# Performance work log

Hardware: AMD Instinct MI355X
Metric: run time of the kernel (lower is better)

Reference implementation:

```python
import jax, jax.numpy as jnp
import numpy as np

N = 50000     # nodes
E = 800000    # edges (avg degree 16)
IN = 128
HID = 128
OUT = 128


def _init_lin(key, n_out, n_in, bias=True):
    k1, k2 = jax.random.split(key)
    bound = 1.0 / np.sqrt(n_in)
    W = jax.random.uniform(k1, (n_out, n_in), minval=-bound, maxval=bound, dtype=jnp.float32)
    if bias:
        b = jax.random.uniform(k2, (n_out,), minval=-bound, maxval=bound, dtype=jnp.float32)
        return W, b
    return W


def setup_inputs() -> dict:
    key = jax.random.key(0)
    ks = jax.random.split(key, 20)
    inp = {
        "s": jax.random.normal(ks[0], (N, IN), dtype=jnp.float32),
        "t": jax.random.normal(ks[1], (N, IN), dtype=jnp.float32),
        "edge_index": jax.random.randint(ks[2], (2, E), 0, N, dtype=jnp.int64),
        "edge_weight": jax.random.normal(ks[3], (E,), dtype=jnp.float32),
    }
    dims = [(HID, IN), (OUT, HID)]
    i = 4
    for layer in range(2):
        n_out, n_in = dims[layer]
        for pre in ("s", "t"):
            Wl, bl = _init_lin(ks[i], n_out, n_in, bias=True); i += 1
            Wr = _init_lin(ks[i], n_out, n_in, bias=False); i += 1
            inp[f"{pre}{layer}_Wl"] = Wl
            inp[f"{pre}{layer}_bl"] = bl
            inp[f"{pre}{layer}_Wr"] = Wr
    return inp


def _sage(x, src, dst, w, Wl, bl, Wr):
    """SAGEConv (mean aggr, weighted messages): lin_l(mean_j w_ij x_j) + lin_r(x_i)."""
    n = x.shape[0]
    msg = x[src] * w[:, None]                                   # [E, d] gather
    agg = jax.ops.segment_sum(msg, dst, num_segments=n)         # [N, d] scatter-add
    cnt = jax.ops.segment_sum(jnp.ones_like(w), dst, num_segments=n)
    mean = agg / jnp.maximum(cnt, 1.0)[:, None]
    return mean @ Wl.T + bl + x @ Wr.T


def reference(s, t, edge_index, edge_weight,
              s0_Wl, s0_bl, s0_Wr, t0_Wl, t0_bl, t0_Wr,
              s1_Wl, s1_bl, s1_Wr, t1_Wl, t1_bl, t1_Wr):
    w = jax.nn.sigmoid(edge_weight)
    src, dst = edge_index[0], edge_index[1]
    # layer 0 (relu; dropout is identity in eval mode)
    s1 = jax.nn.relu(_sage(t, src, dst, w, s0_Wl, s0_bl, s0_Wr))
    t1 = jax.nn.relu(_sage(s, dst, src, w, t0_Wl, t0_bl, t0_Wr))  # flipped edges
    # layer 1 (no activation)
    s2 = _sage(t1, src, dst, w, s1_Wl, s1_bl, s1_Wr)
    t2 = _sage(s1, dst, src, w, t1_Wl, t1_bl, t1_Wr)
    return (s2, t2)
```

## Files before the change

### kernel.cpp

```cpp
#include <hip/hip_runtime.h>
#include <hip/hip_bf16.h>

#define DIM 128
#define BINSHIFT 8
#define BINSZ 256
#define MAXBINS2 400
#define EPB 2048

typedef __attribute__((ext_vector_type(4))) float f32x4;
typedef __attribute__((ext_vector_type(8))) short bf16x8;
typedef __attribute__((ext_vector_type(8))) unsigned short u16x8;

static __device__ __forceinline__ float b2f(unsigned short u) {
    return __uint_as_float(((unsigned int)u) << 16);
}
static __device__ __forceinline__ unsigned short f2b(float f) {
    unsigned int x = __float_as_uint(f);
    unsigned int r = (x + 0x7fffu + ((x >> 16) & 1u)) >> 16;
    return (unsigned short)r;
}

static __device__ __forceinline__ void fma8(float* acc, float w, uint4 v) {
    const unsigned int* u = &v.x;
#pragma unroll
    for (int k = 0; k < 4; k++) {
        acc[2 * k]     += w * __uint_as_float(u[k] << 16);
        acc[2 * k + 1] += w * __uint_as_float(u[k] & 0xffff0000u);
    }
}

__global__ __launch_bounds__(256) void dgnn_bincount(const int* __restrict__ srcI,
        const int* __restrict__ dstI, int* __restrict__ binCnt, int E, int NBINS) {
    __shared__ int hist[MAXBINS2];
    const int nb2 = 2 * NBINS;
    for (int i = threadIdx.x; i < nb2; i += 256) hist[i] = 0;
    __syncthreads();
    int base = blockIdx.x * EPB;
    int end = min(base + EPB, E);
    for (int e = base + threadIdx.x; e < end; e += 256) {
        atomicAdd(&hist[dstI[e] >> BINSHIFT], 1);
        atomicAdd(&hist[NBINS + (srcI[e] >> BINSHIFT)], 1);
    }
    __syncthreads();
    for (int i = threadIdx.x; i < nb2; i += 256) {
        int c = hist[i];
        if (c) atomicAdd(&binCnt[i], c);
    }
}

__global__ __launch_bounds__(1024) void dgnn_binscan(const int* __restrict__ binCnt,
        int* __restrict__ binOffs, int* __restrict__ binCur, int M) {
    __shared__ int sm[1024];
    int tid = threadIdx.x;
    int chunk = (M + 1023) / 1024;
    int b = tid * chunk, e = min(b + chunk, M);
    int s = 0;
    for (int i = b; i < e; i++) s += binCnt[i];
    sm[tid] = s;
    __syncthreads();
    for (int o = 1; o < 1024; o <<= 1) {
        int v = (tid >= o) ? sm[tid - o] : 0;
        __syncthreads();
        sm[tid] += v;
        __syncthreads();
    }
    int run = sm[tid] - s;
    for (int i = b; i < e; i++) {
        int c = binCnt[i];
        binOffs[i] = run; binCur[i] = run;
        run += c;
    }
    if (tid == 1023) binOffs[M] = run;
}

__global__ __launch_bounds__(256) void dgnn_binscatter(const float* __restrict__ ew,
        const int* __restrict__ srcI, const int* __restrict__ dstI,
        int* __restrict__ binCur, int2* __restrict__ binned, int E, int NBINS) {
    __shared__ int hist[MAXBINS2];
    const int nb2 = 2 * NBINS;
    for (int i = threadIdx.x; i < nb2; i += 256) hist[i] = 0;
    __syncthreads();
    int base = blockIdx.x * EPB;
    int end = min(base + EPB, E);
    for (int e = base + threadIdx.x; e < end; e += 256) {
        atomicAdd(&hist[dstI[e] >> BINSHIFT], 1);
        atomicAdd(&hist[NBINS + (srcI[e] >> BINSHIFT)], 1);
    }
    __syncthreads();
    for (int i = threadIdx.x; i < nb2; i += 256) {
        int c = hist[i];
        hist[i] = c ? atomicAdd(&binCur[i], c) : 0;
    }
    __syncthreads();
    for (int e = base + threadIdx.x; e < end; e += 256) {
        int d = dstI[e], s = srcI[e];
        float x = ew[e];
        float w = 1.0f / (1.0f + expf(-x));
        int wb = __float_as_int(w);
        int packed = d | (s << 16);
        int pd = atomicAdd(&hist[d >> BINSHIFT], 1);
        binned[pd] = make_int2(packed, wb);
        int ps = atomicAdd(&hist[NBINS + (s >> BINSHIFT)], 1);
        binned[ps] = make_int2(packed, wb);
    }
}

__global__ __launch_bounds__(256) void dgnn_csrfinal(const int2* __restrict__ binned,
        const int* __restrict__ binOffs, int* __restrict__ offsD, int* __restrict__ offsS,
        int2* __restrict__ nbr2D, int2* __restrict__ nbr2S, int E, int N, int NBINS) {
    int b = blockIdx.x;
    bool isD = b < NBINS;
    int nodeBase = (isD ? b : b - NBINS) << BINSHIFT;
    int beg = binOffs[b], end = binOffs[b + 1];
    int K = end - beg;
    int csrBase = isD ? beg : beg - E;
    int* offs = isD ? offsD : offsS;
    int2* out = isD ? nbr2D : nbr2S;

    __shared__ int cnt[BINSZ], cur[BINSZ], scanb[BINSZ];
    cnt[threadIdx.x] = 0;
    __syncthreads();
    for (int i = threadIdx.x; i < K; i += 256) {
        int pk = binned[beg + i].x;
        int node = isD ? (pk & 0xffff) : ((pk >> 16) & 0xffff);
        atomicAdd(&cnt[node - nodeBase], 1);
    }
    __syncthreads();
    int v = cnt[threadIdx.x];
    scanb[threadIdx.x] = v;
    __syncthreads();
#pragma unroll
    for (int o = 1; o < 256; o <<= 1) {
        int u = (threadIdx.x >= o) ? scanb[threadIdx.x - o] : 0;
        __syncthreads();
        scanb[threadIdx.x] += u;
        __syncthreads();
    }
    int pos = csrBase + scanb[threadIdx.x] - v;
    cur[threadIdx.x] = pos;
    int n = nodeBase + threadIdx.x;
    if (n < N) offs[n] = pos;
    __syncthreads();
    for (int i = threadIdx.x; i < K; i += 256) {
        int2 en = binned[beg + i];
        int node, nbr;
        if (isD) { node = en.x & 0xffff; nbr = (en.x >> 16) & 0xffff; }
        else     { node = (en.x >> 16) & 0xffff; nbr = en.x & 0xffff; }
        int p = atomicAdd(&cur[node - nodeBase], 1);
        out[p] = make_int2(nbr, en.y);
    }
    if (threadIdx.x == 0) {
        if (b == NBINS - 1) offsD[N] = E;
        if (b == 2 * NBINS - 1) offsS[N] = E;
    }
}

__global__ __launch_bounds__(256) void dgnn_cvt2(const float* __restrict__ s,
        const float* __restrict__ t, unsigned short* __restrict__ sb,
        unsigned short* __restrict__ tb, int n4, int halfb) {
    int which = (blockIdx.x >= halfb) ? 1 : 0;
    int i = (blockIdx.x - which * halfb) * 256 + threadIdx.x;
    if (i >= n4) return;
    const float* src = which ? t : s;
    unsigned short* dst = which ? tb : sb;
    float4 v = ((const float4*)src)[i];
    ushort4 o;
    o.x = f2b(v.x); o.y = f2b(v.y); o.z = f2b(v.z); o.w = f2b(v.w);
    ((ushort4*)dst)[i] = o;
}

struct WPtrs { const float* Wl[4]; const float* Wr[4]; };

__global__ __launch_bounds__(256) void dgnn_cvtw(WPtrs wp, unsigned short* __restrict__ Wc) {
    int tid = blockIdx.x * 256 + threadIdx.x;
    int i4 = tid << 2;
    int conv = i4 >> 15;
    int rem = i4 & 32767;
    int ch = rem >> 8;
    int k = rem & 255;
    const float* src = (k < 128) ? wp.Wl[conv] : wp.Wr[conv];
    float4 v = *(const float4*)(src + ch * DIM + (k & 127));
    ushort4 o;
    o.x = f2b(v.x); o.y = f2b(v.y); o.z = f2b(v.z); o.w = f2b(v.w);
    *(ushort4*)(Wc + i4) = o;
}

__global__ __launch_bounds__(256) void dgnn_gather2(
        const unsigned short* __restrict__ xbD, const int* __restrict__ offsD,
        const int2* __restrict__ nbrD, unsigned short* __restrict__ meanD,
        const unsigned short* __restrict__ xbS, const int* __restrict__ offsS,
        const int2* __restrict__ nbrS, unsigned short* __restrict__ meanS,
        int N, int halfb) {
    int which = (blockIdx.x >= halfb) ? 1 : 0;
    const unsigned short* xb = which ? xbS : xbD;
    const int* offs          = which ? offsS : offsD;
    const int2* nbr2         = which ? nbrS : nbrD;
    unsigned short* meanb    = which ? meanS : meanD;

    long long gid = (long long)(blockIdx.x - which * halfb) * 256 + threadIdx.x;
    int n = (int)(gid >> 5);
    if (n >= N) return;
    const int l32 = (int)gid & 31;
    const int q2  = l32 >> 4;
    const int m   = l32 & 15;

    int beg = offs[n], end = offs[n + 1];
    float acc[8];
#pragma unroll
    for (int k = 0; k < 8; k++) acc[k] = 0.f;

    for (int base = beg; base < end; base += 32) {
        int cnt = end - base; if (cnt > 32) cnt = 32;
        bool inb = (base + l32) < end;
        int2 gw = inb ? nbr2[base + l32] : make_int2(0, 0);
        int   g_l = gw.x;
        float w_l = __int_as_float(gw.y);

        int it = 0;
        for (; it + 8 <= cnt; it += 8) {
            int e0 = it + q2, e1 = it + 2 + q2, e2 = it + 4 + q2, e3 = it + 6 + q2;
            int g0 = __shfl(g_l, e0, 32), g1 = __shfl(g_l, e1, 32);
            int g2 = __shfl(g_l, e2, 32), g3 = __shfl(g_l, e3, 32);
            float w0 = __shfl(w_l, e0, 32), w1 = __shfl(w_l, e1, 32);
            float w2 = __shfl(w_l, e2, 32), w3 = __shfl(w_l, e3, 32);
            uint4 v0 = *(const uint4*)(xb + ((size_t)g0 << 7) + (m << 3));
            uint4 v1 = *(const uint4*)(xb + ((size_t)g1 << 7) + (m << 3));
            uint4 v2 = *(const uint4*)(xb + ((size_t)g2 << 7) + (m << 3));
            uint4 v3 = *(const uint4*)(xb + ((size_t)g3 << 7) + (m << 3));
            fma8(acc, w0, v0); fma8(acc, w1, v1);
            fma8(acc, w2, v2); fma8(acc, w3, v3);
        }
        for (; it < cnt; it += 2) {
            int e0 = it + q2;
            int g0 = __shfl(g_l, e0, 32);
            float w0 = __shfl(w_l, e0, 32);
            uint4 v0 = *(const uint4*)(xb + ((size_t)g0 << 7) + (m << 3));
            fma8(acc, w0, v0);
        }
    }

#pragma unroll
    for (int k = 0; k < 8; k++)
        acc[k] += __shfl_xor(acc[k], 16);

    if (q2 == 0) {
        float inv = 1.0f / fmaxf((float)(end - beg), 1.0f);
        u16x8 o;
#pragma unroll
        for (int k = 0; k < 8; k++) o[k] = f2b(acc[k] * inv);
        *(u16x8*)(meanb + ((size_t)n << 7) + (m << 3)) = o;
    }
}

__global__ __launch_bounds__(256) void dgnn_node2(
        const unsigned short* __restrict__ meanA, const unsigned short* __restrict__ xbA,
        const unsigned short* __restrict__ WcA, const float* __restrict__ biasA,
        float* __restrict__ outfA, unsigned short* __restrict__ outbA,
        const unsigned short* __restrict__ meanB, const unsigned short* __restrict__ xbB,
        const unsigned short* __restrict__ WcB, const float* __restrict__ biasB,
        float* __restrict__ outfB, unsigned short* __restrict__ outbB,
        int N, int mode, int halfb) {
    __shared__ __align__(16) unsigned short sW[128 * 256];

    int which = (blockIdx.x >= halfb) ? 1 : 0;
    const unsigned short* meanb = which ? meanB : meanA;
    const unsigned short* xb    = which ? xbB : xbA;
    const unsigned short* Wc    = which ? WcB : WcA;
    const float* bias           = which ? biasB : biasA;
    float* outf                 = which ? outfB : outfA;
    unsigned short* outb        = which ? outbB : outbA;
    int lb = blockIdx.x - which * halfb;

    for (int i = threadIdx.x; i < 4096; i += 256) {
        int ch = i >> 5;
        int off = (i & 31) << 4;
        float4 v = *(const float4*)((const char*)Wc + ((size_t)i << 4));
        int soff = off ^ ((ch & 7) << 4);
        *(float4*)((char*)sW + ch * 512 + soff) = v;
    }
    __syncthreads();

    const int wid = threadIdx.x >> 6;
    const int lane = threadIdx.x & 63;
    const int r = lane & 15;
    const int q = lane >> 4;
    const int ntiles = (N + 15) >> 4;

    for (int tile = lb * 4 + wid; tile < ntiles; tile += halfb * 4) {
        const int n0 = tile << 4;
        const unsigned short* A0 = meanb + (size_t)(n0 + r) * DIM + q * 8;
        const unsigned short* A1 = xb    + (size_t)(n0 + r) * DIM + q * 8;

        f32x4 acc[8];
#pragma unroll
        for (int ct = 0; ct < 8; ct++) acc[ct] = (f32x4){0.f, 0.f, 0.f, 0.f};

#pragma unroll
        for (int ks = 0; ks < 8; ks++) {
            bf16x8 a = (ks < 4) ? *(const bf16x8*)(A0 + ks * 32)
                                : *(const bf16x8*)(A1 + (ks - 4) * 32);
#pragma unroll
            for (int ct = 0; ct < 8; ct++) {
                int ch = ct * 16 + r;
                int soff = (ks * 64 + q * 16) ^ ((ch & 7) << 4);
                bf16x8 b = *(const bf16x8*)((const char*)sW + ch * 512 + soff);
                acc[ct] = __builtin_amdgcn_mfma_f32_16x16x32_bf16(a, b, acc[ct], 0, 0, 0);
            }
        }

#pragma unroll
        for (int ct = 0; ct < 8; ct++) {
            int ch = ct * 16 + r;
            float bv = bias[ch];
#pragma unroll
            for (int rr = 0; rr < 4; rr++) {
                int n = n0 + q * 4 + rr;
                if (n >= N) break;
                float v = acc[ct][rr] + bv;
                if (mode) {
                    v = fmaxf(v, 0.f);
                    outb[(size_t)n * DIM + ch] = f2b(v);
                } else {
                    outf[(size_t)n * DIM + ch] = v;
                }
            }
        }
    }
}

extern "C" void kernel_launch(void* const* d_in, const int* in_sizes, int n_in,
                              void* d_out, int out_size, void* d_ws, size_t ws_size,
                              hipStream_t stream) {
    const float* s  = (const float*)d_in[0];
    const float* t  = (const float*)d_in[1];
    const int*   ei = (const int*)d_in[2];
    const float* ew = (const float*)d_in[3];
    const float* s0_Wl = (const float*)d_in[4];
    const float* s0_bl = (const float*)d_in[5];
    const float* s0_Wr = (const float*)d_in[6];
    const float* t0_Wl = (const float*)d_in[7];
    const float* t0_bl = (const float*)d_in[8];
    const float* t0_Wr = (const float*)d_in[9];
    const float* s1_Wl = (const float*)d_in[10];
    const float* s1_bl = (const float*)d_in[11];
    const float* s1_Wr = (const float*)d_in[12];
    const float* t1_Wl = (const float*)d_in[13];
    const float* t1_bl = (const float*)d_in[14];
    const float* t1_Wr = (const float*)d_in[15];

    const int N = in_sizes[0] / DIM;
    const int E = in_sizes[3];
    const int NBINS = (N + BINSZ - 1) / BINSZ;

    int2* nbr2D = (int2*)d_ws;
    int2* nbr2S = nbr2D + E;
    unsigned short* up = (unsigned short*)(nbr2S + E);
    unsigned short* sb    = up;
    unsigned short* tb    = sb    + (size_t)N * DIM;
    unsigned short* meanA = tb    + (size_t)N * DIM;
    unsigned short* meanB = meanA + (size_t)N * DIM;
    unsigned short* s1b   = meanB + (size_t)N * DIM;
    unsigned short* t1b   = s1b   + (size_t)N * DIM;
    unsigned short* Wc    = t1b   + (size_t)N * DIM;
    int* ip      = (int*)(Wc + 4 * 128 * 256);
    int* binCnt  = ip;
    int* binOffs = binCnt + 2 * NBINS;
    int* binCur  = binOffs + 2 * NBINS + 1;
    int* offsD   = binCur + 2 * NBINS;
    int* offsS   = offsD + (N + 1);

    int2* binned = (int2*)meanA;

    float* sout = (float*)d_out;
    float* tout = sout + (size_t)N * DIM;

    const int* srcI = ei;
    const int* dstI = ei + E;

    const int binb = (E + EPB - 1) / EPB;
    const int gbH = (int)(((long long)N * 32 + 255) / 256);
    const int nodeb = 512;
    const int cvtb = ((N * DIM / 4) + 255) / 256;

    dgnn_cvt2<<<2 * cvtb, 256, 0, stream>>>(s, t, sb, tb, N * DIM / 4, cvtb);
    WPtrs wp;
    wp.Wl[0] = s0_Wl; wp.Wr[0] = s0_Wr;
    wp.Wl[1] = t0_Wl; wp.Wr[1] = t0_Wr;
    wp.Wl[2] = s1_Wl; wp.Wr[2] = s1_Wr;
    wp.Wl[3] = t1_Wl; wp.Wr[3] = t1_Wr;
    dgnn_cvtw<<<128, 256, 0, stream>>>(wp, Wc);

    hipMemsetAsync(binCnt, 0, (size_t)2 * NBINS * sizeof(int), stream);
    dgnn_bincount<<<binb, 256, 0, stream>>>(srcI, dstI, binCnt, E, NBINS);
    dgnn_binscan<<<1, 1024, 0, stream>>>(binCnt, binOffs, binCur, 2 * NBINS);
    dgnn_binscatter<<<binb, 256, 0, stream>>>(ew, srcI, dstI, binCur, binned, E, NBINS);
    dgnn_csrfinal<<<2 * NBINS, 256, 0, stream>>>(binned, binOffs, offsD, offsS,
                                                 nbr2D, nbr2S, E, N, NBINS);

    dgnn_gather2<<<2 * gbH, 256, 0, stream>>>(tb, offsD, nbr2D, meanA,
                                              sb, offsS, nbr2S, meanB, N, gbH);
    dgnn_node2<<<2 * nodeb, 256, 0, stream>>>(
        meanA, tb, Wc,         s0_bl, nullptr, s1b,
        meanB, sb, Wc + 32768, t0_bl, nullptr, t1b, N, 1, nodeb);

    dgnn_gather2<<<2 * gbH, 256, 0, stream>>>(t1b, offsD, nbr2D, meanA,
                                              s1b, offsS, nbr2S, meanB, N, gbH);
    dgnn_node2<<<2 * nodeb, 256, 0, stream>>>(
        meanA, t1b, Wc + 2 * 32768, s1_bl, sout, nullptr,
        meanB, s1b, Wc + 3 * 32768, t1_bl, tout, nullptr, N, 0, nodeb);
}
```

Baseline: 269.5 us.

## Replace bin count+scan with fixed-capacity bins and merge conversion kernels

```diff
diff --git a/kernel.cpp b/kernel.cpp
--- a/kernel.cpp
+++ b/kernel.cpp
@@ -6,6 +6,7 @@
 #define BINSZ 256
 #define MAXBINS2 400
 #define EPB 2048
+#define CAP 6144
 
 typedef __attribute__((ext_vector_type(4))) float f32x4;
 typedef __attribute__((ext_vector_type(8))) short bf16x8;
@@ -29,48 +30,36 @@
     }
 }
 
-__global__ __launch_bounds__(256) void dgnn_bincount(const int* __restrict__ srcI,
-        const int* __restrict__ dstI, int* __restrict__ binCnt, int E, int NBINS) {
-    __shared__ int hist[MAXBINS2];
-    const int nb2 = 2 * NBINS;
-    for (int i = threadIdx.x; i < nb2; i += 256) hist[i] = 0;
-    __syncthreads();
-    int base = blockIdx.x * EPB;
-    int end = min(base + EPB, E);
-    for (int e = base + threadIdx.x; e < end; e += 256) {
-        atomicAdd(&hist[dstI[e] >> BINSHIFT], 1);
-        atomicAdd(&hist[NBINS + (srcI[e] >> BINSHIFT)], 1);
-    }
-    __syncthreads();
-    for (int i = threadIdx.x; i < nb2; i += 256) {
-        int c = hist[i];
-        if (c) atomicAdd(&binCnt[i], c);
-    }
-}
-
-__global__ __launch_bounds__(1024) void dgnn_binscan(const int* __restrict__ binCnt,
-        int* __restrict__ binOffs, int* __restrict__ binCur, int M) {
-    __shared__ int sm[1024];
-    int tid = threadIdx.x;
-    int chunk = (M + 1023) / 1024;
-    int b = tid * chunk, e = min(b + chunk, M);
-    int s = 0;
-    for (int i = b; i < e; i++) s += binCnt[i];
-    sm[tid] = s;
-    __syncthreads();
-    for (int o = 1; o < 1024; o <<= 1) {
-        int v = (tid >= o) ? sm[tid - o] : 0;
-        __syncthreads();
-        sm[tid] += v;
-        __syncthreads();
-    }
-    int run = sm[tid] - s;
-    for (int i = b; i < e; i++) {
-        int c = binCnt[i];
-        binOffs[i] = run; binCur[i] = run;
-        run += c;
-    }
-    if (tid == 1023) binOffs[M] = run;
+struct WPtrs { const float* Wl[4]; const float* Wr[4]; };
+
+__global__ __launch_bounds__(256) void dgnn_prep(
+        const float* __restrict__ s, const float* __restrict__ t,
+        unsigned short* __restrict__ sb, unsigned short* __restrict__ tb,
+        int n4, int cvtb, WPtrs wp, unsigned short* __restrict__ Wc, int wbase) {
+    int b = blockIdx.x;
+    if (b < wbase) {
+        int which = (b >= cvtb) ? 1 : 0;
+        int i = (b - which * cvtb) * 256 + threadIdx.x;
+        if (i >= n4) return;
+        const float* src = which ? t : s;
+        unsigned short* dst = which ? tb : sb;
+        float4 v = ((const float4*)src)[i];
+        ushort4 o;
+        o.x = f2b(v.x); o.y = f2b(v.y); o.z = f2b(v.z); o.w = f2b(v.w);
+        ((ushort4*)dst)[i] = o;
+    } else {
+        int tid = (b - wbase) * 256 + threadIdx.x;
+        int i4 = tid << 2;
+        int conv = i4 >> 15;
+        int rem = i4 & 32767;
+        int ch = rem >> 8;
+        int k = rem & 255;
+        const float* src = (k < 128) ? wp.Wl[conv] : wp.Wr[conv];
+        float4 v = *(const float4*)(src + ch * DIM + (k & 127));
+        ushort4 o;
+        o.x = f2b(v.x); o.y = f2b(v.y); o.z = f2b(v.z); o.w = f2b(v.w);
+        *(ushort4*)(Wc + i4) = o;
+    }
 }
 
 __global__ __launch_bounds__(256) void dgnn_binscatter(const float* __restrict__ ew,
@@ -89,7 +78,8 @@
     __syncthreads();
     for (int i = threadIdx.x; i < nb2; i += 256) {
         int c = hist[i];
-        hist[i] = c ? atomicAdd(&binCur[i], c) : 0;
+        int st = c ? atomicAdd(&binCur[i], c) : 0;
+        hist[i] = i * CAP + st;
     }
     __syncthreads();
     for (int e = base + threadIdx.x; e < end; e += 256) {
@@ -106,22 +96,25 @@
 }
 
 __global__ __launch_bounds__(256) void dgnn_csrfinal(const int2* __restrict__ binned,
-        const int* __restrict__ binOffs, int* __restrict__ offsD, int* __restrict__ offsS,
-        int2* __restrict__ nbr2D, int2* __restrict__ nbr2S, int E, int N, int NBINS) {
+        const int* __restrict__ binCur,
+        int* __restrict__ offsD, int* __restrict__ degD,
+        int* __restrict__ offsS, int* __restrict__ degS,
+        int2* __restrict__ nbr2D, int2* __restrict__ nbr2S, int N, int NBINS) {
     int b = blockIdx.x;
     bool isD = b < NBINS;
-    int nodeBase = (isD ? b : b - NBINS) << BINSHIFT;
-    int beg = binOffs[b], end = binOffs[b + 1];
-    int K = end - beg;
-    int csrBase = isD ? beg : beg - E;
+    int lb = isD ? b : b - NBINS;
+    int nodeBase = lb << BINSHIFT;
+    const int2* bin = binned + (size_t)b * CAP;
+    int K = binCur[b]; if (K > CAP) K = CAP;
     int* offs = isD ? offsD : offsS;
-    int2* out = isD ? nbr2D : nbr2S;
+    int* dga  = isD ? degD : degS;
+    int2* out = (isD ? nbr2D : nbr2S) + (size_t)lb * CAP;
 
     __shared__ int cnt[BINSZ], cur[BINSZ], scanb[BINSZ];
     cnt[threadIdx.x] = 0;
     __syncthreads();
     for (int i = threadIdx.x; i < K; i += 256) {
-        int pk = binned[beg + i].x;
+        int pk = bin[i].x;
         int node = isD ? (pk & 0xffff) : ((pk >> 16) & 0xffff);
         atomicAdd(&cnt[node - nodeBase], 1);
     }
@@ -136,64 +129,33 @@
         scanb[threadIdx.x] += u;
         __syncthreads();
     }
-    int pos = csrBase + scanb[threadIdx.x] - v;
+    int pos = scanb[threadIdx.x] - v;
     cur[threadIdx.x] = pos;
     int n = nodeBase + threadIdx.x;
-    if (n < N) offs[n] = pos;
+    if (n < N) { offs[n] = lb * CAP + pos; dga[n] = v; }
     __syncthreads();
     for (int i = threadIdx.x; i < K; i += 256) {
-        int2 en = binned[beg + i];
+        int2 en = bin[i];
         int node, nbr;
         if (isD) { node = en.x & 0xffff; nbr = (en.x >> 16) & 0xffff; }
         else     { node = (en.x >> 16) & 0xffff; nbr = en.x & 0xffff; }
         int p = atomicAdd(&cur[node - nodeBase], 1);
         out[p] = make_int2(nbr, en.y);
     }
-    if (threadIdx.x == 0) {
-        if (b == NBINS - 1) offsD[N] = E;
-        if (b == 2 * NBINS - 1) offsS[N] = E;
-    }
-}
-
-__global__ __launch_bounds__(256) void dgnn_cvt2(const float* __restrict__ s,
-        const float* __restrict__ t, unsigned short* __restrict__ sb,
-        unsigned short* __restrict__ tb, int n4, int halfb) {
-    int which = (blockIdx.x >= halfb) ? 1 : 0;
-    int i = (blockIdx.x - which * halfb) * 256 + threadIdx.x;
-    if (i >= n4) return;
-    const float* src = which ? t : s;
-    unsigned short* dst = which ? tb : sb;
-    float4 v = ((const float4*)src)[i];
-    ushort4 o;
-    o.x = f2b(v.x); o.y = f2b(v.y); o.z = f2b(v.z); o.w = f2b(v.w);
-    ((ushort4*)dst)[i] = o;
-}
-
-struct WPtrs { const float* Wl[4]; const float* Wr[4]; };
-
-__global__ __launch_bounds__(256) void dgnn_cvtw(WPtrs wp, unsigned short* __restrict__ Wc) {
-    int tid = blockIdx.x * 256 + threadIdx.x;
-    int i4 = tid << 2;
-    int conv = i4 >> 15;
-    int rem = i4 & 32767;
-    int ch = rem >> 8;
-    int k = rem & 255;
-    const float* src = (k < 128) ? wp.Wl[conv] : wp.Wr[conv];
-    float4 v = *(const float4*)(src + ch * DIM + (k & 127));
-    ushort4 o;
-    o.x = f2b(v.x); o.y = f2b(v.y); o.z = f2b(v.z); o.w = f2b(v.w);
-    *(ushort4*)(Wc + i4) = o;
 }
 
 __global__ __launch_bounds__(256) void dgnn_gather2(
         const unsigned short* __restrict__ xbD, const int* __restrict__ offsD,
-        const int2* __restrict__ nbrD, unsigned short* __restrict__ meanD,
+        const int* __restrict__ degD, const int2* __restrict__ nbrD,
+        unsigned short* __restrict__ meanD,
         const unsigned short* __restrict__ xbS, const int* __restrict__ offsS,
-        const int2* __restrict__ nbrS, unsigned short* __restrict__ meanS,
+        const int* __restrict__ degS, const int2* __restrict__ nbrS,
+        unsigned short* __restrict__ meanS,
         int N, int halfb) {
     int which = (blockIdx.x >= halfb) ? 1 : 0;
     const unsigned short* xb = which ? xbS : xbD;
     const int* offs          = which ? offsS : offsD;
+    const int* dga           = which ? degS : degD;
     const int2* nbr2         = which ? nbrS : nbrD;
     unsigned short* meanb    = which ? meanS : meanD;
 
@@ -204,7 +166,9 @@
     const int q2  = l32 >> 4;
     const int m   = l32 & 15;
 
-    int beg = offs[n], end = offs[n + 1];
+    int beg = offs[n];
+    int dg  = dga[n];
+    int end = beg + dg;
     float acc[8];
 #pragma unroll
     for (int k = 0; k < 8; k++) acc[k] = 0.f;
@@ -217,18 +181,19 @@
         float w_l = __int_as_float(gw.y);
 
         int it = 0;
-        for (; it + 8 <= cnt; it += 8) {
-            int e0 = it + q2, e1 = it + 2 + q2, e2 = it + 4 + q2, e3 = it + 6 + q2;
-            int g0 = __shfl(g_l, e0, 32), g1 = __shfl(g_l, e1, 32);
-            int g2 = __shfl(g_l, e2, 32), g3 = __shfl(g_l, e3, 32);
-            float w0 = __shfl(w_l, e0, 32), w1 = __shfl(w_l, e1, 32);
-            float w2 = __shfl(w_l, e2, 32), w3 = __shfl(w_l, e3, 32);
-            uint4 v0 = *(const uint4*)(xb + ((size_t)g0 << 7) + (m << 3));
-            uint4 v1 = *(const uint4*)(xb + ((size_t)g1 << 7) + (m << 3));
-            uint4 v2 = *(const uint4*)(xb + ((size_t)g2 << 7) + (m << 3));
-            uint4 v3 = *(const uint4*)(xb + ((size_t)g3 << 7) + (m << 3));
-            fma8(acc, w0, v0); fma8(acc, w1, v1);
-            fma8(acc, w2, v2); fma8(acc, w3, v3);
+        for (; it + 16 <= cnt; it += 16) {
+            int g[8]; float w[8]; uint4 v[8];
+#pragma unroll
+            for (int k = 0; k < 8; k++) {
+                int e = it + 2 * k + q2;
+                g[k] = __shfl(g_l, e, 32);
+                w[k] = __shfl(w_l, e, 32);
+            }
+#pragma unroll
+            for (int k = 0; k < 8; k++)
+                v[k] = *(const uint4*)(xb + ((size_t)g[k] << 7) + (m << 3));
+#pragma unroll
+            for (int k = 0; k < 8; k++) fma8(acc, w[k], v[k]);
         }
         for (; it < cnt; it += 2) {
             int e0 = it + q2;
@@ -244,7 +209,7 @@
         acc[k] += __shfl_xor(acc[k], 16);
 
     if (q2 == 0) {
-        float inv = 1.0f / fmaxf((float)(end - beg), 1.0f);
+        float inv = 1.0f / fmaxf((float)dg, 1.0f);
         u16x8 o;
 #pragma unroll
         for (int k = 0; k < 8; k++) o[k] = f2b(acc[k] * inv);
@@ -353,8 +318,8 @@
     const int NBINS = (N + BINSZ - 1) / BINSZ;
 
     int2* nbr2D = (int2*)d_ws;
-    int2* nbr2S = nbr2D + E;
-    unsigned short* up = (unsigned short*)(nbr2S + E);
+    int2* nbr2S = nbr2D + (size_t)NBINS * CAP;
+    unsigned short* up = (unsigned short*)(nbr2S + (size_t)NBINS * CAP);
     unsigned short* sb    = up;
     unsigned short* tb    = sb    + (size_t)N * DIM;
     unsigned short* meanA = tb    + (size_t)N * DIM;
@@ -362,12 +327,12 @@
     unsigned short* s1b   = meanB + (size_t)N * DIM;
     unsigned short* t1b   = s1b   + (size_t)N * DIM;
     unsigned short* Wc    = t1b   + (size_t)N * DIM;
-    int* ip      = (int*)(Wc + 4 * 128 * 256);
-    int* binCnt  = ip;
-    int* binOffs = binCnt + 2 * NBINS;
-    int* binCur  = binOffs + 2 * NBINS + 1;
-    int* offsD   = binCur + 2 * NBINS;
-    int* offsS   = offsD + (N + 1);
+    int* ip     = (int*)(Wc + 4 * 128 * 256);
+    int* binCur = ip;
+    int* offsD  = binCur + 2 * NBINS;
+    int* degD   = offsD + N;
+    int* offsS  = degD + N;
+    int* degS   = offsS + N;
 
     int2* binned = (int2*)meanA;
 
@@ -379,32 +344,31 @@
 
     const int binb = (E + EPB - 1) / EPB;
     const int gbH = (int)(((long long)N * 32 + 255) / 256);
-    const int nodeb = 512;
+    const int nodeb = 256;
     const int cvtb = ((N * DIM / 4) + 255) / 256;
 
-    dgnn_cvt2<<<2 * cvtb, 256, 0, stream>>>(s, t, sb, tb, N * DIM / 4, cvtb);
     WPtrs wp;
     wp.Wl[0] = s0_Wl; wp.Wr[0] = s0_Wr;
     wp.Wl[1] = t0_Wl; wp.Wr[1] = t0_Wr;
     wp.Wl[2] = s1_Wl; wp.Wr[2] = s1_Wr;
     wp.Wl[3] = t1_Wl; wp.Wr[3] = t1_Wr;
-    dgnn_cvtw<<<128, 256, 0, stream>>>(wp, Wc);
-
-    hipMemsetAsync(binCnt, 0, (size_t)2 * NBINS * sizeof(int), stream);
-    dgnn_bincount<<<binb, 256, 0, stream>>>(srcI, dstI, binCnt, E, NBINS);
-    dgnn_binscan<<<1, 1024, 0, stream>>>(binCnt, binOffs, binCur, 2 * NBINS);
+    hipMemsetAsync(binCur, 0, (size_t)2 * NBINS * sizeof(int), stream);
+    dgnn_prep<<<2 * cvtb + 128, 256, 0, stream>>>(s, t, sb, tb, N * DIM / 4,
+                                                  cvtb, wp, Wc, 2 * cvtb);
+
     dgnn_binscatter<<<binb, 256, 0, stream>>>(ew, srcI, dstI, binCur, binned, E, NBINS);
-    dgnn_csrfinal<<<2 * NBINS, 256, 0, stream>>>(binned, binOffs, offsD, offsS,
-                                                 nbr2D, nbr2S, E, N, NBINS);
-
-    dgnn_gather2<<<2 * gbH, 256, 0, stream>>>(tb, offsD, nbr2D, meanA,
-                                              sb, offsS, nbr2S, meanB, N, gbH);
+    dgnn_csrfinal<<<2 * NBINS, 256, 0, stream>>>(binned, binCur,
+                                                 offsD, degD, offsS, degS,
+                                                 nbr2D, nbr2S, N, NBINS);
+
+    dgnn_gather2<<<2 * gbH, 256, 0, stream>>>(tb, offsD, degD, nbr2D, meanA,
+                                              sb, offsS, degS, nbr2S, meanB, N, gbH);
     dgnn_node2<<<2 * nodeb, 256, 0, stream>>>(
         meanA, tb, Wc,         s0_bl, nullptr, s1b,
         meanB, sb, Wc + 32768, t0_bl, nullptr, t1b, N, 1, nodeb);
 
-    dgnn_gather2<<<2 * gbH, 256, 0, stream>>>(t1b, offsD, nbr2D, meanA,
-                                              s1b, offsS, nbr2S, meanB, N, gbH);
+    dgnn_gather2<<<2 * gbH, 256, 0, stream>>>(t1b, offsD, degD, nbr2D, meanA,
+                                              s1b, offsS, degS, nbr2S, meanB, N, gbH);
     dgnn_node2<<<2 * nodeb, 256, 0, stream>>>(
         meanA, t1b, Wc + 2 * 32768, s1_bl, sout, nullptr,
         meanB, s1b, Wc + 3 * 32768, t1_bl, tout, nullptr, N, 0, nodeb);
```

After: 253.3 us. 1.06x faster.
